# Kernel tuning notes

Measured on AMD Instinct MI355X. Metric: run time of the kernel, lower is better.

The kernel has to match this reference:

```python
import jax, jax.numpy as jnp
import numpy as np


def _mish(x):
    # mish(x) = x * tanh(softplus(x))
    return x * jnp.tanh(jax.nn.softplus(x))


def setup_inputs() -> dict:
    key = jax.random.key(0)
    k1, k2, k3 = jax.random.split(key, 3)
    x = jax.random.normal(k1, (128, 3, 256, 256), dtype=jnp.float32)
    weight = jax.random.normal(k2, (16, 3, 3, 3), dtype=jnp.float32) * 0.1
    bias = jax.random.normal(k3, (16,), dtype=jnp.float32) * 0.1
    return {"x": x, "weight": weight, "bias": bias}


def reference(x, weight, bias):
    # Valid conv2d (stride 1, no padding), NCHW / OIHW layout
    y = jax.lax.conv_general_dilated(
        x, weight,
        window_strides=(1, 1),
        padding='VALID',
        dimension_numbers=('NCHW', 'OIHW', 'NCHW'))
    y = y + bias[None, :, None, None]
    # two Mish activations
    return _mish(_mish(y))
```

## Files before the change

kernel.cpp:

```cpp
#include <hip/hip_runtime.h>

#define N_  128
#define IC_ 3
#define OC_ 16
#define H_  256
#define W_  256
#define OH_ 254
#define OW_ 254

typedef float v2f __attribute__((ext_vector_type(2)));

__device__ __forceinline__ v2f mish2(v2f x) {
    v2f xe = x * 1.44269504088896340f;
    v2f e;
    e.x = __builtin_amdgcn_exp2f(xe.x);
    e.y = __builtin_amdgcn_exp2f(xe.y);
    v2f p = e + 1.0f;
    v2f t = p * p;
    v2f clampv = {1e30f, 1e30f};
    t = __builtin_elementwise_min(t, clampv);
    v2f num = (t - 1.0f) * x;
    v2f den = t + 1.0f;
    v2f r;
    r.x = __builtin_amdgcn_rcpf(den.x);
    r.y = __builtin_amdgcn_rcpf(den.y);
    return num * r;
}

__global__ void repack_w(const float* __restrict__ w, float* __restrict__ pw) {
    int i = threadIdx.x;
    if (i < 432) {
        int oc = i / 27;
        int r  = i - oc * 27;
        pw[r * 16 + oc] = w[i];
    }
}

__global__ __launch_bounds__(256) void conv_mish_kernel(
    const float* __restrict__ x, const float* __restrict__ pw,
    const float* __restrict__ bias, float* __restrict__ out)
{
    int t    = threadIdx.x;
    int p    = t & 127;
    int row2 = t >> 7;
    int oh   = blockIdx.x * 2 + row2;
    int n    = blockIdx.y;
    if (p >= 127) return;
    int ow0  = p * 2;

    v2f acc0[8], acc1[8];
    const v2f* bq = (const v2f*)bias;
    #pragma unroll
    for (int q = 0; q < 8; ++q) { v2f b = bq[q]; acc0[q] = b; acc1[q] = b; }

    const float* xb = x + (size_t)n * (IC_ * H_ * W_);
    const v2f*   wv = (const v2f*)pw;

    #pragma unroll 1
    for (int s = 0; s < 9; ++s) {
        int ic = s / 3;
        int kh = s - ic * 3;
        const float* rowp = xb + ic * (H_ * W_) + (oh + kh) * W_ + ow0;
        float2 a  = *(const float2*)(rowp);
        float2 b2 = *(const float2*)(rowp + 2);
        float in[4] = {a.x, a.y, b2.x, b2.y};
        #pragma unroll
        for (int kw = 0; kw < 3; ++kw) {
            v2f iv0 = {in[kw],     in[kw]};
            v2f iv1 = {in[kw + 1], in[kw + 1]};
            #pragma unroll
            for (int q = 0; q < 8; ++q) {
                v2f w2 = wv[s * 24 + kw * 8 + q];
                acc0[q] += w2 * iv0;
                acc1[q] += w2 * iv1;
            }
        }
    }

    float* ob = out + (size_t)n * (OC_ * OH_ * OW_) + (size_t)oh * OW_ + ow0;
    #pragma unroll
    for (int q = 0; q < 8; ++q) {
        v2f v0 = mish2(mish2(acc0[q]));
        v2f v1 = mish2(mish2(acc1[q]));
        v2f s0 = {v0.x, v1.x};
        v2f s1 = {v0.y, v1.y};
        __builtin_nontemporal_store(s0, (v2f*)(ob + (size_t)(2 * q)     * (OH_ * OW_)));
        __builtin_nontemporal_store(s1, (v2f*)(ob + (size_t)(2 * q + 1) * (OH_ * OW_)));
    }
}

extern "C" void kernel_launch(void* const* d_in, const int* in_sizes, int n_in,
                              void* d_out, int out_size, void* d_ws, size_t ws_size,
                              hipStream_t stream) {
    const float* x = (const float*)d_in[0];
    const float* w = (const float*)d_in[1];
    const float* b = (const float*)d_in[2];
    float* pw = (float*)d_ws;
    repack_w<<<dim3(1), dim3(512), 0, stream>>>(w, pw);
    dim3 grid(OH_ / 2, N_);
    dim3 block(256);
    conv_mish_kernel<<<grid, block, 0, stream>>>(x, pw, b, (float*)d_out);
}
```

Baseline: 604.3 us.

## Compute four output columns per thread and prefetch next input row

Each thread now accumulates four output columns instead of two, so every weight load is reused across more FMAs. One wave covers one output row with 64 lanes, and the block spans four rows. The input row loads are software-prefetched one step ahead of the accumulation loop to hide global load latency. The cost is more accumulator registers (64 floats), which may lower occupancy, plus a clamped edge load and a masked store for the last lane.

```diff
diff --git a/kernel.cpp b/kernel.cpp
--- a/kernel.cpp
+++ b/kernel.cpp
@@ -40,52 +40,70 @@
     const float* __restrict__ x, const float* __restrict__ pw,
     const float* __restrict__ bias, float* __restrict__ out)
 {
-    int t    = threadIdx.x;
-    int p    = t & 127;
-    int row2 = t >> 7;
-    int oh   = blockIdx.x * 2 + row2;
-    int n    = blockIdx.y;
-    if (p >= 127) return;
-    int ow0  = p * 2;
+    int t  = threadIdx.x;
+    int l  = t & 63;
+    int wv_ = t >> 6;
+    int oh = blockIdx.x * 4 + wv_;
+    if (oh >= OH_) return;
+    int n  = blockIdx.y;
+    int c0 = 4 * l;
+    int c4 = (l == 63) ? 248 : c0 + 4;
 
-    v2f acc0[8], acc1[8];
+    v2f acc[4][8];
     const v2f* bq = (const v2f*)bias;
     #pragma unroll
-    for (int q = 0; q < 8; ++q) { v2f b = bq[q]; acc0[q] = b; acc1[q] = b; }
+    for (int q = 0; q < 8; ++q) {
+        v2f b = bq[q];
+        acc[0][q] = b; acc[1][q] = b; acc[2][q] = b; acc[3][q] = b;
+    }
 
     const float* xb = x + (size_t)n * (IC_ * H_ * W_);
-    const v2f*   wv = (const v2f*)pw;
+    const v2f*   wt = (const v2f*)pw;
+
+    const float* rp0 = xb + (size_t)oh * W_;
+    float4 a  = *(const float4*)(rp0 + c0);
+    float2 b2 = *(const float2*)(rp0 + c4);
 
     #pragma unroll 1
     for (int s = 0; s < 9; ++s) {
-        int ic = s / 3;
-        int kh = s - ic * 3;
-        const float* rowp = xb + ic * (H_ * W_) + (oh + kh) * W_ + ow0;
-        float2 a  = *(const float2*)(rowp);
-        float2 b2 = *(const float2*)(rowp + 2);
-        float in[4] = {a.x, a.y, b2.x, b2.y};
+        float in0 = a.x, in1 = a.y, in2 = a.z, in3 = a.w, in4 = b2.x, in5 = b2.y;
+        if (s < 8) {
+            int s1 = s + 1;
+            int ic = s1 / 3, kh = s1 - ic * 3;
+            const float* rp = xb + ic * (H_ * W_) + (size_t)(oh + kh) * W_;
+            a  = *(const float4*)(rp + c0);
+            b2 = *(const float2*)(rp + c4);
+        }
+        float in[6] = {in0, in1, in2, in3, in4, in5};
         #pragma unroll
         for (int kw = 0; kw < 3; ++kw) {
-            v2f iv0 = {in[kw],     in[kw]};
-            v2f iv1 = {in[kw + 1], in[kw + 1]};
             #pragma unroll
             for (int q = 0; q < 8; ++q) {
-                v2f w2 = wv[s * 24 + kw * 8 + q];
-                acc0[q] += w2 * iv0;
-                acc1[q] += w2 * iv1;
+                v2f w2 = wt[s * 24 + kw * 8 + q];
+                acc[0][q] += w2 * (v2f){in[kw + 0], in[kw + 0]};
+                acc[1][q] += w2 * (v2f){in[kw + 1], in[kw + 1]};
+                acc[2][q] += w2 * (v2f){in[kw + 2], in[kw + 2]};
+                acc[3][q] += w2 * (v2f){in[kw + 3], in[kw + 3]};
             }
         }
     }
 
-    float* ob = out + (size_t)n * (OC_ * OH_ * OW_) + (size_t)oh * OW_ + ow0;
+    float* ob = out + (size_t)n * (OC_ * OH_ * OW_) + (size_t)oh * OW_ + c0;
+    bool hi_ok = (l < 63);
     #pragma unroll
     for (int q = 0; q < 8; ++q) {
-        v2f v0 = mish2(mish2(acc0[q]));
-        v2f v1 = mish2(mish2(acc1[q]));
-        v2f s0 = {v0.x, v1.x};
-        v2f s1 = {v0.y, v1.y};
-        __builtin_nontemporal_store(s0, (v2f*)(ob + (size_t)(2 * q)     * (OH_ * OW_)));
-        __builtin_nontemporal_store(s1, (v2f*)(ob + (size_t)(2 * q + 1) * (OH_ * OW_)));
+        v2f m0 = mish2(mish2(acc[0][q]));
+        v2f m1 = mish2(mish2(acc[1][q]));
+        v2f m2 = mish2(mish2(acc[2][q]));
+        v2f m3 = mish2(mish2(acc[3][q]));
+        float* p0 = ob + (size_t)(2 * q)     * (OH_ * OW_);
+        float* p1 = ob + (size_t)(2 * q + 1) * (OH_ * OW_);
+        __builtin_nontemporal_store((v2f){m0.x, m1.x}, (v2f*)p0);
+        __builtin_nontemporal_store((v2f){m0.y, m1.y}, (v2f*)p1);
+        if (hi_ok) {
+            __builtin_nontemporal_store((v2f){m2.x, m3.x}, (v2f*)(p0 + 2));
+            __builtin_nontemporal_store((v2f){m2.y, m3.y}, (v2f*)(p1 + 2));
+        }
     }
 }
 
@@ -97,7 +115,7 @@
     const float* b = (const float*)d_in[2];
     float* pw = (float*)d_ws;
     repack_w<<<dim3(1), dim3(512), 0, stream>>>(w, pw);
-    dim3 grid(OH_ / 2, N_);
+    dim3 grid((OH_ + 3) / 4, N_);
     dim3 block(256);
     conv_mish_kernel<<<grid, block, 0, stream>>>(x, pw, b, (float*)d_out);
 }
```

Result: slower. 823.2 us (+36.2%).
